# Optimization experiments

Hardware: AMD Instinct MI355X
Metric: run time of the kernel (lower is better)

Reference implementation:

```python
import jax, jax.numpy as jnp
import numpy as np

DECAY = 0.9        # membrane leak per step
THRESH = 1.0       # spike threshold
SLOPE = 4.0        # fast-sigmoid surrogate slope
W_SCALE = 0.01     # weight init scale to keep dynamics sane


def _spike_fn(v):
    # Heaviside forward, fast-sigmoid surrogate backward (straight-through).
    s = jax.nn.sigmoid(SLOPE * (v - THRESH))
    h = (v > THRESH).astype(v.dtype)
    return jax.lax.stop_gradient(h - s) + s


def setup_inputs() -> dict:
    key = jax.random.key(0)
    ks = jax.random.split(key, 6)
    T, B, NE, NI = 64, 32, 4096, 1024
    return {
        "ext_exc": jax.random.normal(ks[0], (T, B, NE), dtype=jnp.float32),
        "ext_inh": jax.random.normal(ks[1], (T, B, NI), dtype=jnp.float32),
        "W_ee": jax.random.normal(ks[2], (NE, NE), dtype=jnp.float32) * W_SCALE,
        "W_ei": jax.random.normal(ks[3], (NI, NE), dtype=jnp.float32) * W_SCALE,
        "W_ie": jax.random.normal(ks[4], (NE, NI), dtype=jnp.float32) * W_SCALE,
        "W_ii": jax.random.normal(ks[5], (NI, NI), dtype=jnp.float32) * W_SCALE,
        "time_steps": 64,
    }


def reference(ext_exc, ext_inh, W_ee, W_ei, W_ie, W_ii, time_steps):
    B, NE = ext_exc.shape[1], ext_exc.shape[2]
    NI = ext_inh.shape[2]
    dt = ext_exc.dtype
    v_e = jnp.zeros((B, NE), dt)
    v_i = jnp.zeros((B, NI), dt)
    s_e = jnp.zeros((B, NE), dt)
    s_i = jnp.zeros((B, NI), dt)

    def step(carry, xs):
        v_e, v_i, s_e, s_i = carry
        ie_ext, ii_ext = xs
        # recurrent currents from PREVIOUS step spikes (matches current_spikes semantics)
        i_e = ie_ext + s_e @ W_ee.T + s_i @ W_ie.T
        i_i = ii_ext + s_e @ W_ei.T + s_i @ W_ii.T
        # LIF update: leak + integrate, spike, hard reset
        v_e = v_e * DECAY + i_e
        v_i = v_i * DECAY + i_i
        ns_e = _spike_fn(v_e)
        ns_i = _spike_fn(v_i)
        v_e = v_e * (1.0 - ns_e)
        v_i = v_i * (1.0 - ns_i)
        return (v_e, v_i, ns_e, ns_i), (ns_e, ns_i)

    xs = (ext_exc[:time_steps], ext_inh[:time_steps])
    _, (hist_e, hist_i) = jax.lax.scan(step, (v_e, v_i, s_e, s_i), xs)
    # spike_history as one array: [T, B, NE+NI] (exc then inh populations)
    return jnp.concatenate([hist_e, hist_i], axis=-1)
```

## Files before the change

kernel.cpp:

```cpp
#include <hip/hip_runtime.h>


#define NE 4096
#define NI 1024
#define NN 5120
#define HN 2560
#define BB 32
#define CHUNK 64

typedef unsigned int u32;

__device__ __forceinline__ void load_lds16(const float* g, float* l) {
    __builtin_amdgcn_global_load_lds(
        (const __attribute__((address_space(1))) u32*)g,
        (__attribute__((address_space(3))) u32*)l, 16, 0, 0);
}

__global__ __launch_bounds__(256) void pack_kernel(
    const float* __restrict__ out_t, u32* __restrict__ mask)
{
    const int n = blockIdx.x * 256 + threadIdx.x;
    u32 m = 0;
#pragma unroll
    for (int b = 0; b < BB; ++b)
        m |= (out_t[(size_t)b * NN + n] > 0.5f ? 1u : 0u) << b;
    mask[n] = m;
}

template <int KR>
__global__ __launch_bounds__(256) void mv_kernel(
    const float* __restrict__ W_ee, const float* __restrict__ W_ei,
    const float* __restrict__ W_ie, const float* __restrict__ W_ii,
    const u32* __restrict__ mask,
    double* __restrict__ partial)
{
    __shared__ __align__(16) float tile[16 * 128 * 4];
    const int t    = threadIdx.x;
    const int lane = t & 63;
    const int wv   = t >> 6;
    const int jh   = wv << 3;
    const int nA   = blockIdx.x * 64 + lane;
    const int kb0  = blockIdx.y * KR;

    const int n0 = blockIdx.x * 64;
    const int n1 = n0 + HN;
    const bool h1E = (n1 < NE);
    const float* e0 = W_ee + (size_t)n0 * NE;
    const float* e1 = h1E ? (W_ee + (size_t)n1 * NE) : (W_ei + (size_t)(n1 - NE) * NE);
    const float* i0 = W_ie + (size_t)n0 * NI;
    const float* i1 = h1E ? (W_ie + (size_t)n1 * NI) : (W_ii + (size_t)(n1 - NE) * NI);

    double accA[8], accB[8];
#pragma unroll
    for (int j = 0; j < 8; ++j) { accA[j] = 0.0; accB[j] = 0.0; }

    for (int ch = 0; ch < KR / CHUNK; ++ch) {
        const int kb = kb0 + ch * CHUNK;
        const bool eseg = (kb < NE);
        const int kloc = eseg ? kb : kb - NE;
        const size_t kdim = eseg ? NE : NI;
        const float* b0 = eseg ? e0 : i0;
        const float* b1 = eseg ? e1 : i1;

        if (ch) __syncthreads();
#pragma unroll
        for (int c = 0; c < 8; ++c) {
            const int slot = wv * 8 + c;
            const int q = slot >> 1;
            const float* base = (slot & 1) ? b1 : b0;
            const float* gsrc = base + (size_t)lane * kdim + (kloc + q * 4);
            load_lds16(gsrc, &tile[slot * 256]);
        }
        __syncthreads();

#pragma unroll 4
        for (int q = 0; q < 16; ++q) {
            const float4 wa = *reinterpret_cast<const float4*>(&tile[(q * 128 + lane) * 4]);
            const float4 wb = *reinterpret_cast<const float4*>(&tile[(q * 128 + 64 + lane) * 4]);
            const uint4 mq = *reinterpret_cast<const uint4*>(&mask[kb + q * 4]);
            const u32 m0 = ((u32)__builtin_amdgcn_readfirstlane(mq.x)) >> jh;
            const u32 m1 = ((u32)__builtin_amdgcn_readfirstlane(mq.y)) >> jh;
            const u32 m2 = ((u32)__builtin_amdgcn_readfirstlane(mq.z)) >> jh;
            const u32 m3 = ((u32)__builtin_amdgcn_readfirstlane(mq.w)) >> jh;

            const double wa0 = (double)wa.x, wa1 = (double)wa.y,
                         wa2 = (double)wa.z, wa3 = (double)wa.w;
            const double wb0 = (double)wb.x, wb1 = (double)wb.y,
                         wb2 = (double)wb.z, wb3 = (double)wb.w;
#pragma unroll
            for (int j = 0; j < 8; ++j) {
                const double s0 = (double)((m0 >> j) & 1u);
                const double s1 = (double)((m1 >> j) & 1u);
                const double s2 = (double)((m2 >> j) & 1u);
                const double s3 = (double)((m3 >> j) & 1u);
                accA[j] += wa0 * s0 + wa1 * s1 + wa2 * s2 + wa3 * s3;
                accB[j] += wb0 * s0 + wb1 * s1 + wb2 * s2 + wb3 * s3;
            }
        }
    }

#pragma unroll
    for (int j = 0; j < 8; ++j) {
        const size_t base = ((size_t)blockIdx.y * BB + jh + j) * NN;
        partial[base + nA] = accA[j];
        partial[base + nA + HN] = accB[j];
    }
}

template <int G>
__global__ __launch_bounds__(256) void upd_kernel(
    const float* __restrict__ ext_exc,
    const float* __restrict__ ext_inh,
    const double* __restrict__ partial,
    double* __restrict__ v,
    float* __restrict__ out,
    int t)
{
    const int idx = blockIdx.x * 256 + threadIdx.x;
    const int b = idx / NN;
    const int n = idx - b * NN;

    const float ext = (n < NE)
        ? ext_exc[((size_t)t * BB + b) * NE + n]
        : ext_inh[((size_t)t * BB + b) * NI + (n - NE)];

    double acc = (double)ext;
#pragma unroll
    for (int g = 0; g < G; ++g)
        acc += partial[((size_t)g * BB + b) * NN + n];

    const double vv = v[idx] * 0.9 + acc;
    const double sp = (vv > 1.0) ? 1.0 : 0.0;
    out[(size_t)t * BB * NN + idx] = (float)sp;
    v[idx] = vv * (1.0 - sp);
}

extern "C" void kernel_launch(void* const* d_in, const int* in_sizes, int n_in,
                              void* d_out, int out_size, void* d_ws, size_t ws_size,
                              hipStream_t stream) {
    const float* ext_exc = (const float*)d_in[0];
    const float* ext_inh = (const float*)d_in[1];
    const float* W_ee = (const float*)d_in[2];
    const float* W_ei = (const float*)d_in[3];
    const float* W_ie = (const float*)d_in[4];
    const float* W_ii = (const float*)d_in[5];
    float* out = (float*)d_out;

    const int T = in_sizes[0] / (BB * NE);

    const size_t SN = (size_t)BB * NN;
    double* v = (double*)d_ws;
    u32* mask = (u32*)(v + SN);
    const size_t stateBytes = SN * 8 + (size_t)NN * 4;
    double* partial = (double*)((char*)d_ws + stateBytes);

    int G = 16;
    if (stateBytes + (size_t)G * SN * sizeof(double) > ws_size) G = 8;

    hipMemsetAsync(d_ws, 0, stateBytes, stream);

    for (int t = 0; t < T; ++t) {
        if (G == 16) {
            mv_kernel<320><<<dim3(HN / 64, 16), 256, 0, stream>>>(
                W_ee, W_ei, W_ie, W_ii, mask, partial);
            upd_kernel<16><<<(int)(SN / 256), 256, 0, stream>>>(
                ext_exc, ext_inh, partial, v, out, t);
        } else {
            mv_kernel<640><<<dim3(HN / 64, 8), 256, 0, stream>>>(
                W_ee, W_ei, W_ie, W_ii, mask, partial);
            upd_kernel<8><<<(int)(SN / 256), 256, 0, stream>>>(
                ext_exc, ext_inh, partial, v, out, t);
        }
        pack_kernel<<<NN / 256, 256, 0, stream>>>(out + (size_t)t * SN, mask);
    }
}
```

Measured before the change: 5.663 ms.

## Fuse matvec, membrane update and spike packing into one per-step kernel

Combines the three per-timestep kernels into a single step kernel. The last block to finish each output column, detected with an atomic counter, reduces the K-split partials, updates membrane state, writes spikes and builds the packed spike mask for the next step. Mask buffers are double-buffered, the K split grows from 16 to 32 groups and the chunk size is halved to add parallelism. This aims to cut launch overhead and the extra passes over the output, at the cost of the serialized last-block reduction and atomic/fence synchronization.

```diff
diff --git a/kernel.cpp b/kernel.cpp
--- a/kernel.cpp
+++ b/kernel.cpp
@@ -6,7 +6,8 @@
 #define NN 5120
 #define HN 2560
 #define BB 32
-#define CHUNK 64
+#define CHUNK 32
+#define NCOL 40
 
 typedef unsigned int u32;
 
@@ -16,38 +17,39 @@
         (__attribute__((address_space(3))) u32*)l, 16, 0, 0);
 }
 
-__global__ __launch_bounds__(256) void pack_kernel(
-    const float* __restrict__ out_t, u32* __restrict__ mask)
-{
-    const int n = blockIdx.x * 256 + threadIdx.x;
-    u32 m = 0;
-#pragma unroll
-    for (int b = 0; b < BB; ++b)
-        m |= (out_t[(size_t)b * NN + n] > 0.5f ? 1u : 0u) << b;
-    mask[n] = m;
-}
-
-template <int KR>
-__global__ __launch_bounds__(256) void mv_kernel(
+template <int G>
+__global__ __launch_bounds__(256) void step_kernel(
     const float* __restrict__ W_ee, const float* __restrict__ W_ei,
     const float* __restrict__ W_ie, const float* __restrict__ W_ii,
-    const u32* __restrict__ mask,
-    double* __restrict__ partial)
+    const float* __restrict__ ext_exc,
+    const float* __restrict__ ext_inh,
+    const u32* __restrict__ maskIn,
+    u32* __restrict__ maskOut,
+    double* __restrict__ partial,
+    double* __restrict__ v,
+    float* __restrict__ out,
+    int* __restrict__ cnt,
+    int t)
 {
-    __shared__ __align__(16) float tile[16 * 128 * 4];
-    const int t    = threadIdx.x;
-    const int lane = t & 63;
-    const int wv   = t >> 6;
+    constexpr int KR = NN / G;
+    __shared__ __align__(16) float tile[16 * 256];
+    __shared__ u32 s_m[128];
+    __shared__ int s_won;
+
+    const int tid  = threadIdx.x;
+    const int lane = tid & 63;
+    const int wv   = tid >> 6;
     const int jh   = wv << 3;
-    const int nA   = blockIdx.x * 64 + lane;
-    const int kb0  = blockIdx.y * KR;
+    const int col  = blockIdx.x;
+    const int g    = blockIdx.y;
+    const int nA   = col * 64 + lane;
+    const int kb0  = g * KR;
 
-    const int n0 = blockIdx.x * 64;
-    const int n1 = n0 + HN;
+    const int n1 = col * 64 + HN;
     const bool h1E = (n1 < NE);
-    const float* e0 = W_ee + (size_t)n0 * NE;
+    const float* e0 = W_ee + (size_t)(col * 64) * NE;
     const float* e1 = h1E ? (W_ee + (size_t)n1 * NE) : (W_ei + (size_t)(n1 - NE) * NE);
-    const float* i0 = W_ie + (size_t)n0 * NI;
+    const float* i0 = W_ie + (size_t)(col * 64) * NI;
     const float* i1 = h1E ? (W_ie + (size_t)n1 * NI) : (W_ii + (size_t)(n1 - NE) * NI);
 
     double accA[8], accB[8];
@@ -64,20 +66,20 @@
 
         if (ch) __syncthreads();
 #pragma unroll
-        for (int c = 0; c < 8; ++c) {
-            const int slot = wv * 8 + c;
+        for (int c = 0; c < 4; ++c) {
+            const int slot = wv * 4 + c;
             const int q = slot >> 1;
             const float* base = (slot & 1) ? b1 : b0;
-            const float* gsrc = base + (size_t)lane * kdim + (kloc + q * 4);
-            load_lds16(gsrc, &tile[slot * 256]);
+            load_lds16(base + (size_t)lane * kdim + (kloc + q * 4),
+                       &tile[slot * 256]);
         }
         __syncthreads();
 
-#pragma unroll 4
-        for (int q = 0; q < 16; ++q) {
-            const float4 wa = *reinterpret_cast<const float4*>(&tile[(q * 128 + lane) * 4]);
-            const float4 wb = *reinterpret_cast<const float4*>(&tile[(q * 128 + 64 + lane) * 4]);
-            const uint4 mq = *reinterpret_cast<const uint4*>(&mask[kb + q * 4]);
+#pragma unroll
+        for (int q = 0; q < 8; ++q) {
+            const float4 wa = *reinterpret_cast<const float4*>(&tile[(q * 2 + 0) * 256 + lane * 4]);
+            const float4 wb = *reinterpret_cast<const float4*>(&tile[(q * 2 + 1) * 256 + lane * 4]);
+            const uint4 mq = *reinterpret_cast<const uint4*>(&maskIn[kb + q * 4]);
             const u32 m0 = ((u32)__builtin_amdgcn_readfirstlane(mq.x)) >> jh;
             const u32 m1 = ((u32)__builtin_amdgcn_readfirstlane(mq.y)) >> jh;
             const u32 m2 = ((u32)__builtin_amdgcn_readfirstlane(mq.z)) >> jh;
@@ -101,38 +103,44 @@
 
 #pragma unroll
     for (int j = 0; j < 8; ++j) {
-        const size_t base = ((size_t)blockIdx.y * BB + jh + j) * NN;
+        const size_t base = ((size_t)g * BB + jh + j) * NN;
         partial[base + nA] = accA[j];
         partial[base + nA + HN] = accB[j];
     }
-}
 
-template <int G>
-__global__ __launch_bounds__(256) void upd_kernel(
-    const float* __restrict__ ext_exc,
-    const float* __restrict__ ext_inh,
-    const double* __restrict__ partial,
-    double* __restrict__ v,
-    float* __restrict__ out,
-    int t)
-{
-    const int idx = blockIdx.x * 256 + threadIdx.x;
-    const int b = idx / NN;
-    const int n = idx - b * NN;
+    __threadfence();
+    __syncthreads();
+    if (tid == 0)
+        s_won = (atomicAdd(&cnt[t * NCOL + col], 1) == G - 1) ? 1 : 0;
+    __syncthreads();
+    if (!s_won) return;
+    __threadfence();
 
-    const float ext = (n < NE)
-        ? ext_exc[((size_t)t * BB + b) * NE + n]
-        : ext_inh[((size_t)t * BB + b) * NI + (n - NE)];
+    if (tid < 128) s_m[tid] = 0u;
+    __syncthreads();
 
-    double acc = (double)ext;
+    const int ni = tid & 127;
+    const int n = (ni < 64) ? (col * 64 + ni) : (HN + col * 64 + (ni - 64));
+    u32 mbits = 0;
+    for (int e = tid; e < 4096; e += 256) {
+        const int b = e >> 7;
+        const float ext = (n < NE)
+            ? ext_exc[((size_t)t * BB + b) * NE + n]
+            : ext_inh[((size_t)t * BB + b) * NI + (n - NE)];
+        double acc = (double)ext;
 #pragma unroll
-    for (int g = 0; g < G; ++g)
-        acc += partial[((size_t)g * BB + b) * NN + n];
-
-    const double vv = v[idx] * 0.9 + acc;
-    const double sp = (vv > 1.0) ? 1.0 : 0.0;
-    out[(size_t)t * BB * NN + idx] = (float)sp;
-    v[idx] = vv * (1.0 - sp);
+        for (int g2 = 0; g2 < G; ++g2)
+            acc += partial[((size_t)g2 * BB + b) * NN + n];
+        const size_t vi = (size_t)b * NN + n;
+        const double vv = v[vi] * 0.9 + acc;
+        const double sp = (vv > 1.0) ? 1.0 : 0.0;
+        out[(size_t)t * BB * NN + vi] = (float)sp;
+        v[vi] = vv * (1.0 - sp);
+        if (sp != 0.0) mbits |= (1u << b);
+    }
+    atomicOr(&s_m[ni], mbits);
+    __syncthreads();
+    if (tid < 128) maskOut[n] = s_m[tid];
 }
 
 extern "C" void kernel_launch(void* const* d_in, const int* in_sizes, int n_in,
@@ -150,27 +158,29 @@
 
     const size_t SN = (size_t)BB * NN;
     double* v = (double*)d_ws;
-    u32* mask = (u32*)(v + SN);
-    const size_t stateBytes = SN * 8 + (size_t)NN * 4;
-    double* partial = (double*)((char*)d_ws + stateBytes);
+    u32* maskA = (u32*)(v + SN);
+    u32* maskB = maskA + NN;
+    int* cnt = (int*)(maskB + NN);
+    const size_t stateBytes = SN * 8 + (size_t)NN * 8 + (size_t)T * NCOL * 4;
+    double* partial = (double*)((char*)d_ws + ((stateBytes + 15) & ~(size_t)15));
 
-    int G = 16;
-    if (stateBytes + (size_t)G * SN * sizeof(double) > ws_size) G = 8;
+    const size_t base = ((stateBytes + 15) & ~(size_t)15);
+    int G = 32;
+    if (base + (size_t)G * SN * sizeof(double) > ws_size) G = 16;
 
     hipMemsetAsync(d_ws, 0, stateBytes, stream);
 
     for (int t = 0; t < T; ++t) {
-        if (G == 16) {
-            mv_kernel<320><<<dim3(HN / 64, 16), 256, 0, stream>>>(
-                W_ee, W_ei, W_ie, W_ii, mask, partial);
-            upd_kernel<16><<<(int)(SN / 256), 256, 0, stream>>>(
-                ext_exc, ext_inh, partial, v, out, t);
+        const u32* mIn  = (t & 1) ? maskB : maskA;
+        u32*       mOut = (t & 1) ? maskA : maskB;
+        if (G == 32) {
+            step_kernel<32><<<dim3(NCOL, 32), 256, 0, stream>>>(
+                W_ee, W_ei, W_ie, W_ii, ext_exc, ext_inh,
+                mIn, mOut, partial, v, out, cnt, t);
         } else {
-            mv_kernel<640><<<dim3(HN / 64, 8), 256, 0, stream>>>(
-                W_ee, W_ei, W_ie, W_ii, mask, partial);
-            upd_kernel<8><<<(int)(SN / 256), 256, 0, stream>>>(
-                ext_exc, ext_inh, partial, v, out, t);
+            step_kernel<16><<<dim3(NCOL, 16), 256, 0, stream>>>(
+                W_ee, W_ei, W_ie, W_ii, ext_exc, ext_inh,
+                mIn, mOut, partial, v, out, cnt, t);
         }
-        pack_kernel<<<NN / 256, 256, 0, stream>>>(out + (size_t)t * SN, mask);
     }
 }
```

New measurement: 13.97 ms. 147% more time.
